# Optimization experiments

Hardware: AMD Instinct MI355X
Metric: run time of the kernel (lower is better)

## Reference

```python
import jax, jax.numpy as jnp
import numpy as np

DT = 1.0
EPS = 1e-6


def setup_inputs() -> dict:
    key = jax.random.key(0)
    ks = jax.random.split(key, 5)
    B, I, H = 8192, 512, 1024
    scale = (6.0 / ((1 + 5.0) * (I + H))) ** 0.5  # kaiming_uniform with a=sqrt(5) bound
    return {
        "x": jax.random.normal(ks[0], (B, I), dtype=jnp.float32),
        "hidden": jax.random.normal(ks[1], (B, H), dtype=jnp.float32),
        "W_tau": jax.random.uniform(ks[2], (H, I + H), dtype=jnp.float32, minval=-scale, maxval=scale),
        "b_tau": jnp.zeros((H,), dtype=jnp.float32),
        "W_r": jax.random.uniform(ks[3], (H, I + H), dtype=jnp.float32, minval=-scale, maxval=scale),
        "b_r": jnp.zeros((H,), dtype=jnp.float32),
        "W_h": jax.random.uniform(ks[4], (H, I + H), dtype=jnp.float32, minval=-scale, maxval=scale),
        "b_h": jnp.zeros((H,), dtype=jnp.float32),
    }


def reference(x, hidden, W_tau, b_tau, W_r, b_r, W_h, b_h):
    combined = jnp.concatenate([x, hidden], axis=1)          # [B, I+H]
    tau = jax.nn.softplus(combined @ W_tau.T + b_tau) + EPS  # [B, H]
    r = jax.nn.sigmoid(combined @ W_r.T + b_r)               # [B, H]
    gated = r * hidden
    cand_in = jnp.concatenate([x, gated], axis=1)            # [B, I+H]
    h_tilde = jnp.tanh(cand_in @ W_h.T + b_h)                # [B, H]
    return hidden + DT * (h_tilde - hidden) / tau
```

## Files before the change

### kernel.cpp

```cpp
#include <hip/hip_runtime.h>
#include <hip/hip_bf16.h>

typedef __attribute__((ext_vector_type(8))) unsigned short u16x8;
typedef __attribute__((ext_vector_type(8))) __bf16        bf16x8;
typedef __attribute__((ext_vector_type(4))) float         f32x4;

static constexpr int B_ = 8192;
static constexpr int I_ = 512;
static constexpr int H_ = 1024;
static constexpr int K_ = 1536;
static constexpr int NT    = K_ / 64;
static constexpr int NITER = NT / 2;

#define AS1 __attribute__((address_space(1)))
#define AS3 __attribute__((address_space(3)))

__device__ __forceinline__ unsigned short f2bf(float f) {
    unsigned int u = __float_as_uint(f);
    u += 0x7FFF + ((u >> 16) & 1);
    return (unsigned short)(u >> 16);
}

__device__ __forceinline__ void memfence() { asm volatile("" ::: "memory"); }
__device__ __forceinline__ void barrier_() {
    memfence(); __builtin_amdgcn_s_barrier(); memfence();
}
__device__ __forceinline__ void vwait6() {
    asm volatile("s_waitcnt vmcnt(6)" ::: "memory");
    __builtin_amdgcn_sched_barrier(0);
}
__device__ __forceinline__ void vwait4() {
    asm volatile("s_waitcnt vmcnt(4)" ::: "memory");
    __builtin_amdgcn_sched_barrier(0);
}

__device__ __forceinline__ u16x8 cvt8(const float4* s) {
    float4 a = s[0], b = s[1];
    u16x8 o;
    o[0] = f2bf(a.x); o[1] = f2bf(a.y); o[2] = f2bf(a.z); o[3] = f2bf(a.w);
    o[4] = f2bf(b.x); o[5] = f2bf(b.y); o[6] = f2bf(b.z); o[7] = f2bf(b.w);
    return o;
}

__global__ void prep(const float* __restrict__ x, const float* __restrict__ hid,
                     const float* __restrict__ wt, const float* __restrict__ wr,
                     const float* __restrict__ wh,
                     unsigned short* __restrict__ cmb1,
                     unsigned short* __restrict__ wtb,
                     unsigned short* __restrict__ wrb,
                     unsigned short* __restrict__ whb) {
    constexpr int NX8 = B_ * I_ / 8;
    constexpr int NH8 = B_ * H_ / 8;
    constexpr int NW8 = H_ * K_ / 8;
    int i = blockIdx.x * blockDim.x + threadIdx.x;
    if (i < NX8) {
        int row = i >> 6, c8 = i & 63;
        u16x8 o = cvt8((const float4*)x + (size_t)i * 2);
        *(u16x8*)(cmb1 + (size_t)row * K_ + c8 * 8) = o;
    } else if (i < NX8 + NH8) {
        int j = i - NX8;
        int row = j >> 7, c8 = j & 127;
        u16x8 o = cvt8((const float4*)hid + (size_t)j * 2);
        *(u16x8*)(cmb1 + (size_t)row * K_ + 512 + c8 * 8) = o;
    } else {
        int k = i - (NX8 + NH8);
        const float* src; unsigned short* dst;
        if (k < NW8)          { src = wt; dst = wtb; }
        else if (k < 2 * NW8) { src = wr; dst = wrb; k -= NW8; }
        else                  { src = wh; dst = whb; k -= 2 * NW8; }
        u16x8 o = cvt8((const float4*)src + (size_t)k * 2);
        *(u16x8*)(dst + (size_t)k * 8) = o;
    }
}

__global__ __launch_bounds__(512, 1)
void gemm_tr(const unsigned short* __restrict__ A,
             const unsigned short* __restrict__ W0,
             const unsigned short* __restrict__ W1,
             const float* __restrict__ b0,
             const float* __restrict__ b1,
             const float* __restrict__ hidden,
             unsigned short* __restrict__ itau_out,
             unsigned short* __restrict__ gate_out)
{
    extern __shared__ __align__(16) char lds[];

    const int t = threadIdx.x;
    const int w = t >> 6, l = t & 63;
    const int wg  = blockIdx.y * 8 + blockIdx.x;
    const int swz = (wg & 7) * 32 + (wg >> 3);
    const int m0  = (swz >> 3) * 256;
    const int n0  = (swz & 7) * 128;

    const int srow  = t >> 3;
    const int sslot = ((t & 7) ^ (srow & 7)) * 8;
    const unsigned short* srcA  = A  + (size_t)(m0 + srow) * K_ + sslot;
    const unsigned short* srcB0 = W0 + (size_t)(n0 + srow) * K_ + sslot;
    const unsigned short* srcB1 = W1 + (size_t)(n0 + srow) * K_ + sslot;
    char* dstA = lds + w * 1024;
    char* dstB = lds + 65536 + w * 1024;

    auto stageA = [&](int tt) {
        const unsigned short* s = srcA + tt * 64;
        char* d = dstA + (tt & 1) * 32768;
        #pragma unroll
        for (int q = 0; q < 4; ++q)
            __builtin_amdgcn_global_load_lds(
                (const AS1 void*)(s + (size_t)q * 64 * K_),
                (AS3 void*)(d + q * 8192), 16, 0, 0);
    };
    auto stageB = [&](int tt, int wi) {
        const unsigned short* s = (wi ? srcB1 : srcB0) + tt * 64;
        char* d = dstB + (tt & 1) * 32768 + wi * 16384;
        #pragma unroll
        for (int h = 0; h < 2; ++h)
            __builtin_amdgcn_global_load_lds(
                (const AS1 void*)(s + (size_t)(h * 64) * K_),
                (AS3 void*)(d + h * 8192), 16, 0, 0);
    };

    const int fr = l & 15, kq = l >> 4;
    const int wm = w >> 1, wn = w & 1;
    const int fx = (kq ^ (fr & 7)) << 4;
    const char* rdA0 = lds + (wm * 32 + fr) * 128 + fx;
    const char* rdA1 = lds + (wm * 32 + fr) * 128 + (fx ^ 64);
    const char* rdB0 = lds + 65536 + (wn * 32 + fr) * 128 + fx;
    const char* rdB1 = lds + 65536 + (wn * 32 + fr) * 128 + (fx ^ 64);

    bf16x8 af[4][2], bfr[2][2][2];
    f32x4 acc[2][4][4];
    #pragma unroll
    for (int wi = 0; wi < 2; ++wi)
        #pragma unroll
        for (int i = 0; i < 4; ++i)
            #pragma unroll
            for (int jn = 0; jn < 4; ++jn) acc[wi][i][jn] = (f32x4)0.0f;

    auto readAfull = [&](int par) {
        #pragma unroll
        for (int mf = 0; mf < 4; ++mf) {
            const int off = par * 32768 + (mf >> 1) * 16384 + (mf & 1) * 2048;
            af[mf][0] = *(const bf16x8*)(rdA0 + off);
            af[mf][1] = *(const bf16x8*)(rdA1 + off);
        }
    };
    auto readB = [&](int wi, int par) {
        #pragma unroll
        for (int bh = 0; bh < 2; ++bh)
            #pragma unroll
            for (int ni = 0; ni < 2; ++ni) {
                const int off = par * 32768 + wi * 16384 + bh * 8192 + ni * 2048;
                bfr[bh][ni][0] = *(const bf16x8*)(rdB0 + off);
                bfr[bh][ni][1] = *(const bf16x8*)(rdB1 + off);
            }
    };
    auto mfma32 = [&](int wi) {
        __builtin_amdgcn_s_setprio(1);
        #pragma unroll
        for (int mf = 0; mf < 4; ++mf)
            #pragma unroll
            for (int bh = 0; bh < 2; ++bh)
                #pragma unroll
                for (int ni = 0; ni < 2; ++ni)
                    #pragma unroll
                    for (int ks = 0; ks < 2; ++ks)
                        acc[wi][mf][bh * 2 + ni] =
                            __builtin_amdgcn_mfma_f32_16x16x32_bf16(
                                af[mf][ks], bfr[bh][ni][ks],
                                acc[wi][mf][bh * 2 + ni], 0, 0, 0);
        __builtin_amdgcn_s_setprio(0);
    };

    stageA(0); stageB(0, 0); stageB(0, 1);
    stageA(1); stageB(1, 0);
    vwait6(); barrier_();

    for (int j = 0; j < NITER; ++j) {
        const int tE = (2 * j + 2 < NT) ? 2 * j + 2 : 0;
        const int tO = (2 * j + 3 < NT) ? 2 * j + 3 : 0;
        readAfull(0); readB(0, 0); stageB(2 * j + 1, 1);
        mfma32(0); barrier_();
        readB(1, 0); stageA(tE); stageB(tE, 0);
        mfma32(1); vwait6(); barrier_();
        readAfull(1); readB(0, 1); stageB(tE, 1);
        mfma32(0); barrier_();
        readB(1, 1); stageA(tO); stageB(tO, 0);
        mfma32(1); vwait6(); barrier_();
    }
    asm volatile("s_waitcnt vmcnt(0)" ::: "memory");

    const int rs4 = kq * 4;
    const int nB0 = n0 + wn * 32;
    #pragma unroll
    for (int wi = 0; wi < 2; ++wi)
        #pragma unroll
        for (int mf = 0; mf < 4; ++mf)
            #pragma unroll
            for (int bh = 0; bh < 2; ++bh)
                #pragma unroll
                for (int ni = 0; ni < 2; ++ni) {
                    const int n = nB0 + bh * 64 + ni * 16 + fr;
                    const float bv = (wi ? b1 : b0)[n];
                    #pragma unroll
                    for (int jj = 0; jj < 4; ++jj) {
                        const int m = m0 + (mf >> 1) * 128 + wm * 32 + (mf & 1) * 16 + rs4 + jj;
                        const size_t ix = (size_t)m * H_ + n;
                        const float z = acc[wi][mf][bh * 2 + ni][jj] + bv;
                        if (wi == 0) {
                            const float sp = (z > 15.f) ? z : __logf(1.0f + __expf(z));
                            itau_out[ix] = f2bf(__fdividef(1.0f, sp + 1e-6f));
                        } else {
                            const float r = __fdividef(1.0f, 1.0f + __expf(-z));
                            gate_out[(size_t)m * K_ + 512 + n] = f2bf(r * hidden[ix]);
                        }
                    }
                }
}

__global__ __launch_bounds__(512, 1)
void gemm_h(const unsigned short* __restrict__ A1,
            const unsigned short* __restrict__ A2,
            const unsigned short* __restrict__ W0,
            const float* __restrict__ bias0,
            const float* __restrict__ hidden,
            const unsigned short* __restrict__ itau_in,
            float* __restrict__ outF)
{
    extern __shared__ __align__(16) char lds[];

    const int t = threadIdx.x;
    const int w = t >> 6, l = t & 63;
    const int wg  = blockIdx.y * 8 + blockIdx.x;
    const int swz = (wg & 7) * 32 + (wg >> 3);
    const int m0  = (swz >> 3) * 256;
    const int n0  = (swz & 7) * 128;

    const int srow  = t >> 3;
    const int sslot = ((t & 7) ^ (srow & 7)) * 8;
    const unsigned short* srcA1 = A1 + (size_t)(m0 + srow) * K_ + sslot;
    const unsigned short* srcA2 = A2 + (size_t)(m0 + srow) * K_ + sslot;
    const unsigned short* srcB  = W0 + (size_t)(n0 + srow) * K_ + sslot;
    char* dstA = lds + w * 1024;
    char* dstB = lds + 65536 + w * 1024;

    auto stageA = [&](int tt, int h) {
        const unsigned short* base = (tt >= 8) ? srcA2 : srcA1;
        const unsigned short* s = base + (size_t)(h * 128) * K_ + tt * 64;
        char* d = dstA + (tt & 1) * 32768 + h * 16384;
        #pragma unroll
        for (int j = 0; j < 2; ++j)
            __builtin_amdgcn_global_load_lds(
                (const AS1 void*)(s + (size_t)j * 64 * K_),
                (AS3 void*)(d + j * 8192), 16, 0, 0);
    };
    auto stageB = [&](int tt, int h) {
        const unsigned short* s = srcB + (size_t)(h * 64) * K_ + tt * 64;
        char* d = dstB + (tt & 1) * 16384 + h * 8192;
        __builtin_amdgcn_global_load_lds((const AS1 void*)s, (AS3 void*)d, 16, 0, 0);
    };

    const int fr = l & 15, kq = l >> 4;
    const int wm = w >> 1, wn = w & 1;
    const int fx = (kq ^ (fr & 7)) << 4;
    const char* rdA0 = lds + (wm * 32 + fr) * 128 + fx;
    const char* rdA1 = lds + (wm * 32 + fr) * 128 + (fx ^ 64);
    const char* rdB0 = lds + 65536 + (wn * 32 + fr) * 128 + fx;
    const char* rdB1 = lds + 65536 + (wn * 32 + fr) * 128 + (fx ^ 64);

    bf16x8 af[2][2], bfr[2][2][2];
    f32x4 acc[4][4];
    #pragma unroll
    for (int i = 0; i < 4; ++i)
        #pragma unroll
        for (int jn = 0; jn < 4; ++jn) acc[i][jn] = (f32x4)0.0f;

    auto readA = [&](int half, int par) {
        #pragma unroll
        for (int mi = 0; mi < 2; ++mi) {
            af[mi][0] = *(const bf16x8*)(rdA0 + par * 32768 + half * 16384 + mi * 2048);
            af[mi][1] = *(const bf16x8*)(rdA1 + par * 32768 + half * 16384 + mi * 2048);
        }
    };
    auto readBall = [&](int par) {
        #pragma unroll
        for (int bh = 0; bh < 2; ++bh)
            #pragma unroll
            for (int ni = 0; ni < 2; ++ni) {
                bfr[bh][ni][0] = *(const bf16x8*)(rdB0 + par * 16384 + bh * 8192 + ni * 2048);
                bfr[bh][ni][1] = *(const bf16x8*)(rdB1 + par * 16384 + bh * 8192 + ni * 2048);
            }
    };
    auto quad16 = [&](int ah) {
        __builtin_amdgcn_s_setprio(1);
        #pragma unroll
        for (int bh = 0; bh < 2; ++bh)
            #pragma unroll
            for (int mi = 0; mi < 2; ++mi)
                #pragma unroll
                for (int ni = 0; ni < 2; ++ni)
                    #pragma unroll
                    for (int ks = 0; ks < 2; ++ks)
                        acc[ah * 2 + mi][bh * 2 + ni] =
                            __builtin_amdgcn_mfma_f32_16x16x32_bf16(
                                af[mi][ks], bfr[bh][ni][ks],
                                acc[ah * 2 + mi][bh * 2 + ni], 0, 0, 0);
        __builtin_amdgcn_s_setprio(0);
    };

    stageA(0, 0); stageA(0, 1); stageB(0, 0); stageB(0, 1);
    stageA(1, 0); stageB(1, 0); stageB(1, 1);
    vwait4(); barrier_();

    for (int j = 0; j < NITER; ++j) {
        const int tE = (2 * j + 2 < NT) ? 2 * j + 2 : 0;
        const int tO = (2 * j + 3 < NT) ? 2 * j + 3 : 0;
        readA(0, 0); readBall(0); stageA(2 * j + 1, 1);
        quad16(0); barrier_();
        readA(1, 0); stageA(tE, 0); stageB(tE, 0); stageB(tE, 1);
        quad16(1); vwait4(); barrier_();
        readA(0, 1); readBall(1); stageA(tE, 1);
        quad16(0); barrier_();
        readA(1, 1); stageA(tO, 0); stageB(tO, 0); stageB(tO, 1);
        quad16(1); vwait4(); barrier_();
    }
    asm volatile("s_waitcnt vmcnt(0)" ::: "memory");

    const int rs4 = kq * 4;
    const int nB0 = n0 + wn * 32;
    const int mB0 = m0 + wm * 32;
    #pragma unroll
    for (int ah = 0; ah < 2; ++ah)
        #pragma unroll
        for (int mi = 0; mi < 2; ++mi)
            #pragma unroll
            for (int bh = 0; bh < 2; ++bh)
                #pragma unroll
                for (int ni = 0; ni < 2; ++ni) {
                    const int n = nB0 + bh * 64 + ni * 16 + fr;
                    const float bv = bias0[n];
                    #pragma unroll
                    for (int jj = 0; jj < 4; ++jj) {
                        const int m = mB0 + ah * 128 + mi * 16 + rs4 + jj;
                        const size_t ix = (size_t)m * H_ + n;
                        const float z = acc[ah * 2 + mi][bh * 2 + ni][jj] + bv;
                        const float e2 = __expf(2.0f * z);
                        const float th = __fdividef(e2 - 1.0f, e2 + 1.0f);
                        const float h = hidden[ix];
                        const float it = __uint_as_float(((unsigned)itau_in[ix]) << 16);
                        outF[ix] = h + (th - h) * it;
                    }
                }
}

extern "C" void kernel_launch(void* const* d_in, const int* in_sizes, int n_in,
                              void* d_out, int out_size, void* d_ws, size_t ws_size,
                              hipStream_t stream) {
    (void)in_sizes; (void)n_in; (void)out_size; (void)ws_size;

    const float* x     = (const float*)d_in[0];
    const float* hid   = (const float*)d_in[1];
    const float* W_tau = (const float*)d_in[2];
    const float* b_tau = (const float*)d_in[3];
    const float* W_r   = (const float*)d_in[4];
    const float* b_r   = (const float*)d_in[5];
    const float* W_h   = (const float*)d_in[6];
    const float* b_h   = (const float*)d_in[7];

    unsigned short* cmb1 = (unsigned short*)d_ws;
    unsigned short* cmb2 = cmb1 + (size_t)B_ * K_;
    unsigned short* wtb  = cmb2 + (size_t)B_ * K_;
    unsigned short* wrb  = wtb  + (size_t)H_ * K_;
    unsigned short* whb  = wrb  + (size_t)H_ * K_;
    unsigned short* itau = whb  + (size_t)H_ * K_;

    hipFuncSetAttribute(reinterpret_cast<const void*>(&gemm_tr),
                        hipFuncAttributeMaxDynamicSharedMemorySize, 131072);
    hipFuncSetAttribute(reinterpret_cast<const void*>(&gemm_h),
                        hipFuncAttributeMaxDynamicSharedMemorySize, 98304);

    const int th = 256;
    constexpr int NPREP = B_ * I_ / 8 + B_ * H_ / 8 + 3 * H_ * K_ / 8;
    prep<<<NPREP / th, th, 0, stream>>>(x, hid, W_tau, W_r, W_h,
                                        cmb1, wtb, wrb, whb);

    dim3 g(8, 32);
    gemm_tr<<<g, 512, 131072, stream>>>(cmb1, wtb, wrb, b_tau, b_r, hid,
                                        itau, cmb2);
    gemm_h<<<g, 512, 98304, stream>>>(cmb1, cmb2, whb, b_h, hid, itau,
                                      (float*)d_out);
}
```

Baseline: 105.9 us.

## Retile gemm_h to 128x128 blocks of 256 threads with two blocks per CU

The second GEMM goes from 256x128 tiles with 512 threads and one block per CU to 128x128 tiles with 256 threads, 64 KB of LDS and two blocks per CU, on a 512-block grid. The staged two-tile pipeline is replaced by a simpler double buffer that prefetches the next K tile, then waits for all loads (vmcnt(0)) before the barrier. Each wave now computes a 64x64 sub-tile. The aim is more blocks in flight to hide latency and better wave-count balance, at the cost of less operand reuse per tile and a fully serialising wait each K step.

```diff
diff --git a/kernel.cpp b/kernel.cpp
--- a/kernel.cpp
+++ b/kernel.cpp
@@ -20,6 +20,9 @@
     u += 0x7FFF + ((u >> 16) & 1);
     return (unsigned short)(u >> 16);
 }
+__device__ __forceinline__ float bf2f(unsigned short u) {
+    return __uint_as_float(((unsigned int)u) << 16);
+}
 
 __device__ __forceinline__ void memfence() { asm volatile("" ::: "memory"); }
 __device__ __forceinline__ void barrier_() {
@@ -29,8 +32,8 @@
     asm volatile("s_waitcnt vmcnt(6)" ::: "memory");
     __builtin_amdgcn_sched_barrier(0);
 }
-__device__ __forceinline__ void vwait4() {
-    asm volatile("s_waitcnt vmcnt(4)" ::: "memory");
+__device__ __forceinline__ void vwait0() {
+    asm volatile("s_waitcnt vmcnt(0)" ::: "memory");
     __builtin_amdgcn_sched_barrier(0);
 }
 
@@ -187,7 +190,7 @@
         readB(1, 1); stageA(tO); stageB(tO, 0);
         mfma32(1); vwait6(); barrier_();
     }
-    asm volatile("s_waitcnt vmcnt(0)" ::: "memory");
+    vwait0();
 
     const int rs4 = kq * 4;
     const int nB0 = n0 + wn * 32;
@@ -217,11 +220,11 @@
                 }
 }
 
-__global__ __launch_bounds__(512, 1)
+__global__ __launch_bounds__(256, 2)
 void gemm_h(const unsigned short* __restrict__ A1,
             const unsigned short* __restrict__ A2,
-            const unsigned short* __restrict__ W0,
-            const float* __restrict__ bias0,
+            const unsigned short* __restrict__ W,
+            const float* __restrict__ bias,
             const float* __restrict__ hidden,
             const unsigned short* __restrict__ itau_in,
             float* __restrict__ outF)
@@ -231,125 +234,103 @@
     const int t = threadIdx.x;
     const int w = t >> 6, l = t & 63;
     const int wg  = blockIdx.y * 8 + blockIdx.x;
-    const int swz = (wg & 7) * 32 + (wg >> 3);
-    const int m0  = (swz >> 3) * 256;
+    const int swz = (wg & 7) * 64 + (wg >> 3);
+    const int m0  = (swz >> 3) * 128;
     const int n0  = (swz & 7) * 128;
 
     const int srow  = t >> 3;
     const int sslot = ((t & 7) ^ (srow & 7)) * 8;
     const unsigned short* srcA1 = A1 + (size_t)(m0 + srow) * K_ + sslot;
     const unsigned short* srcA2 = A2 + (size_t)(m0 + srow) * K_ + sslot;
-    const unsigned short* srcB  = W0 + (size_t)(n0 + srow) * K_ + sslot;
-    char* dstA = lds + w * 1024;
-    char* dstB = lds + 65536 + w * 1024;
-
-    auto stageA = [&](int tt, int h) {
-        const unsigned short* base = (tt >= 8) ? srcA2 : srcA1;
-        const unsigned short* s = base + (size_t)(h * 128) * K_ + tt * 64;
-        char* d = dstA + (tt & 1) * 32768 + h * 16384;
-        #pragma unroll
-        for (int j = 0; j < 2; ++j)
+    const unsigned short* srcB  = W  + (size_t)(n0 + srow) * K_ + sslot;
+
+    auto stageTile = [&](int bi, int ts) {
+        const unsigned short* sA = (ts >= 8 ? srcA2 : srcA1) + ts * 64;
+        char* dA = lds + bi * 16384 + w * 1024;
+        #pragma unroll
+        for (int q = 0; q < 4; ++q)
             __builtin_amdgcn_global_load_lds(
-                (const AS1 void*)(s + (size_t)j * 64 * K_),
-                (AS3 void*)(d + j * 8192), 16, 0, 0);
-    };
-    auto stageB = [&](int tt, int h) {
-        const unsigned short* s = srcB + (size_t)(h * 64) * K_ + tt * 64;
-        char* d = dstB + (tt & 1) * 16384 + h * 8192;
-        __builtin_amdgcn_global_load_lds((const AS1 void*)s, (AS3 void*)d, 16, 0, 0);
+                (const AS1 void*)(sA + (size_t)q * 32 * K_),
+                (AS3 void*)(dA + q * 4096), 16, 0, 0);
+        const unsigned short* sB = srcB + ts * 64;
+        char* dB = lds + 32768 + bi * 16384 + w * 1024;
+        #pragma unroll
+        for (int q = 0; q < 4; ++q)
+            __builtin_amdgcn_global_load_lds(
+                (const AS1 void*)(sB + (size_t)q * 32 * K_),
+                (AS3 void*)(dB + q * 4096), 16, 0, 0);
     };
 
     const int fr = l & 15, kq = l >> 4;
     const int wm = w >> 1, wn = w & 1;
     const int fx = (kq ^ (fr & 7)) << 4;
-    const char* rdA0 = lds + (wm * 32 + fr) * 128 + fx;
-    const char* rdA1 = lds + (wm * 32 + fr) * 128 + (fx ^ 64);
-    const char* rdB0 = lds + 65536 + (wn * 32 + fr) * 128 + fx;
-    const char* rdB1 = lds + 65536 + (wn * 32 + fr) * 128 + (fx ^ 64);
-
-    bf16x8 af[2][2], bfr[2][2][2];
+    const char* rdA0 = lds + (wm * 64 + fr) * 128 + fx;
+    const char* rdA1 = lds + (wm * 64 + fr) * 128 + (fx ^ 64);
+    const char* rdB0 = lds + 32768 + (wn * 64 + fr) * 128 + fx;
+    const char* rdB1 = lds + 32768 + (wn * 64 + fr) * 128 + (fx ^ 64);
+
+    bf16x8 af[4][2], bfr[4][2];
     f32x4 acc[4][4];
     #pragma unroll
     for (int i = 0; i < 4; ++i)
         #pragma unroll
         for (int jn = 0; jn < 4; ++jn) acc[i][jn] = (f32x4)0.0f;
 
-    auto readA = [&](int half, int par) {
-        #pragma unroll
-        for (int mi = 0; mi < 2; ++mi) {
-            af[mi][0] = *(const bf16x8*)(rdA0 + par * 32768 + half * 16384 + mi * 2048);
-            af[mi][1] = *(const bf16x8*)(rdA1 + par * 32768 + half * 16384 + mi * 2048);
+    auto readFrags = [&](int bi) {
+        #pragma unroll
+        for (int mf = 0; mf < 4; ++mf) {
+            af[mf][0] = *(const bf16x8*)(rdA0 + bi * 16384 + mf * 2048);
+            af[mf][1] = *(const bf16x8*)(rdA1 + bi * 16384 + mf * 2048);
         }
-    };
-    auto readBall = [&](int par) {
-        #pragma unroll
-        for (int bh = 0; bh < 2; ++bh)
-            #pragma unroll
-            for (int ni = 0; ni < 2; ++ni) {
-                bfr[bh][ni][0] = *(const bf16x8*)(rdB0 + par * 16384 + bh * 8192 + ni * 2048);
-                bfr[bh][ni][1] = *(const bf16x8*)(rdB1 + par * 16384 + bh * 8192 + ni * 2048);
+        #pragma unroll
+        for (int nf = 0; nf < 4; ++nf) {
+            bfr[nf][0] = *(const bf16x8*)(rdB0 + bi * 16384 + nf * 2048);
+            bfr[nf][1] = *(const bf16x8*)(rdB1 + bi * 16384 + nf * 2048);
+        }
+    };
+    auto mfma32 = [&]() {
+        __builtin_amdgcn_s_setprio(1);
+        #pragma unroll
+        for (int mf = 0; mf < 4; ++mf)
+            #pragma unroll
+            for (int nf = 0; nf < 4; ++nf)
+                #pragma unroll
+                for (int ks = 0; ks < 2; ++ks)
+                    acc[mf][nf] = __builtin_amdgcn_mfma_f32_16x16x32_bf16(
+                        af[mf][ks], bfr[nf][ks], acc[mf][nf], 0, 0, 0);
+        __builtin_amdgcn_s_setprio(0);
+    };
+
+    stageTile(0, 0);
+    vwait0(); barrier_();
+
+    for (int ts = 0; ts < NT; ++ts) {
+        const int bi = ts & 1;
+        stageTile(bi ^ 1, (ts + 1 < NT) ? ts + 1 : 0);
+        readFrags(bi);
+        mfma32();
+        vwait0(); barrier_();
+    }
+
+    const int rs4 = kq * 4;
+    #pragma unroll
+    for (int mf = 0; mf < 4; ++mf)
+        #pragma unroll
+        for (int nf = 0; nf < 4; ++nf) {
+            const int n = n0 + wn * 64 + nf * 16 + fr;
+            const float bv = bias[n];
+            #pragma unroll
+            for (int jj = 0; jj < 4; ++jj) {
+                const int m = m0 + wm * 64 + mf * 16 + rs4 + jj;
+                const size_t ix = (size_t)m * H_ + n;
+                const float z = acc[mf][nf][jj] + bv;
+                const float e2 = __expf(2.0f * z);
+                const float th = __fdividef(e2 - 1.0f, e2 + 1.0f);
+                const float h = hidden[ix];
+                const float it = bf2f(itau_in[ix]);
+                outF[ix] = h + (th - h) * it;
             }
-    };
-    auto quad16 = [&](int ah) {
-        __builtin_amdgcn_s_setprio(1);
-        #pragma unroll
-        for (int bh = 0; bh < 2; ++bh)
-            #pragma unroll
-            for (int mi = 0; mi < 2; ++mi)
-                #pragma unroll
-                for (int ni = 0; ni < 2; ++ni)
-                    #pragma unroll
-                    for (int ks = 0; ks < 2; ++ks)
-                        acc[ah * 2 + mi][bh * 2 + ni] =
-                            __builtin_amdgcn_mfma_f32_16x16x32_bf16(
-                                af[mi][ks], bfr[bh][ni][ks],
-                                acc[ah * 2 + mi][bh * 2 + ni], 0, 0, 0);
-        __builtin_amdgcn_s_setprio(0);
-    };
-
-    stageA(0, 0); stageA(0, 1); stageB(0, 0); stageB(0, 1);
-    stageA(1, 0); stageB(1, 0); stageB(1, 1);
-    vwait4(); barrier_();
-
-    for (int j = 0; j < NITER; ++j) {
-        const int tE = (2 * j + 2 < NT) ? 2 * j + 2 : 0;
-        const int tO = (2 * j + 3 < NT) ? 2 * j + 3 : 0;
-        readA(0, 0); readBall(0); stageA(2 * j + 1, 1);
-        quad16(0); barrier_();
-        readA(1, 0); stageA(tE, 0); stageB(tE, 0); stageB(tE, 1);
-        quad16(1); vwait4(); barrier_();
-        readA(0, 1); readBall(1); stageA(tE, 1);
-        quad16(0); barrier_();
-        readA(1, 1); stageA(tO, 0); stageB(tO, 0); stageB(tO, 1);
-        quad16(1); vwait4(); barrier_();
-    }
-    asm volatile("s_waitcnt vmcnt(0)" ::: "memory");
-
-    const int rs4 = kq * 4;
-    const int nB0 = n0 + wn * 32;
-    const int mB0 = m0 + wm * 32;
-    #pragma unroll
-    for (int ah = 0; ah < 2; ++ah)
-        #pragma unroll
-        for (int mi = 0; mi < 2; ++mi)
-            #pragma unroll
-            for (int bh = 0; bh < 2; ++bh)
-                #pragma unroll
-                for (int ni = 0; ni < 2; ++ni) {
-                    const int n = nB0 + bh * 64 + ni * 16 + fr;
-                    const float bv = bias0[n];
-                    #pragma unroll
-                    for (int jj = 0; jj < 4; ++jj) {
-                        const int m = mB0 + ah * 128 + mi * 16 + rs4 + jj;
-                        const size_t ix = (size_t)m * H_ + n;
-                        const float z = acc[ah * 2 + mi][bh * 2 + ni][jj] + bv;
-                        const float e2 = __expf(2.0f * z);
-                        const float th = __fdividef(e2 - 1.0f, e2 + 1.0f);
-                        const float h = hidden[ix];
-                        const float it = __uint_as_float(((unsigned)itau_in[ix]) << 16);
-                        outF[ix] = h + (th - h) * it;
-                    }
-                }
+        }
 }
 
 extern "C" void kernel_launch(void* const* d_in, const int* in_sizes, int n_in,
@@ -376,16 +357,17 @@
     hipFuncSetAttribute(reinterpret_cast<const void*>(&gemm_tr),
                         hipFuncAttributeMaxDynamicSharedMemorySize, 131072);
     hipFuncSetAttribute(reinterpret_cast<const void*>(&gemm_h),
-                        hipFuncAttributeMaxDynamicSharedMemorySize, 98304);
+                        hipFuncAttributeMaxDynamicSharedMemorySize, 65536);
 
     const int th = 256;
     constexpr int NPREP = B_ * I_ / 8 + B_ * H_ / 8 + 3 * H_ * K_ / 8;
     prep<<<NPREP / th, th, 0, stream>>>(x, hid, W_tau, W_r, W_h,
                                         cmb1, wtb, wrb, whb);
 
-    dim3 g(8, 32);
-    gemm_tr<<<g, 512, 131072, stream>>>(cmb1, wtb, wrb, b_tau, b_r, hid,
-                                        itau, cmb2);
-    gemm_h<<<g, 512, 98304, stream>>>(cmb1, cmb2, whb, b_h, hid, itau,
-                                      (float*)d_out);
-}
+    dim3 g0(8, 32);
+    gemm_tr<<<g0, 512, 131072, stream>>>(cmb1, wtb, wrb, b_tau, b_r, hid,
+                                         itau, cmb2);
+    dim3 g1(8, 64);
+    gemm_h<<<g1, 256, 65536, stream>>>(cmb1, cmb2, whb, b_h, hid, itau,
+                                       (float*)d_out);
+}
```

After: 106.1 us, median of 2. About the same (+0.2%).
